# Kernel tuning notes

Measured on AMD Instinct MI355X. Metric: run time of the kernel, lower is better.

## Reference

```python
import math
import jax, jax.numpy as jnp
import numpy as np

B, CIN, Hh, Ww = 8, 3, 64, 64
D_MODEL = 512
N_STATE = 64
N2 = N_STATE // 2
N_LAYERS = 4
LATENT = 256
L = Hh * Ww  # 4096
EPS = 1e-5


def setup_inputs() -> dict:
    key = jax.random.key(0)
    ks = jax.random.split(key, 12)
    x = jax.random.normal(ks[0], (B, CIN, Hh, Ww), jnp.float32)
    Wproj = jax.random.normal(ks[1], (D_MODEL, CIN), jnp.float32) * (1.0 / math.sqrt(CIN))
    bproj = jnp.zeros((D_MODEL,), jnp.float32)
    pos_emb = jax.random.normal(ks[2], (1, L, D_MODEL), jnp.float32)
    # S4D kernel params (stacked over layers), per minimal S4D init
    log_dt = jax.random.uniform(ks[3], (N_LAYERS, D_MODEL), jnp.float32) * (math.log(0.1) - math.log(0.001)) + math.log(0.001)
    log_A_real = jnp.full((N_LAYERS, D_MODEL, N2), math.log(0.5), jnp.float32)
    A_imag = jnp.broadcast_to(math.pi * jnp.arange(N2, dtype=jnp.float32), (N_LAYERS, D_MODEL, N2)) + jnp.zeros((N_LAYERS, D_MODEL, N2), jnp.float32)
    C_re = jax.random.normal(ks[4], (N_LAYERS, D_MODEL, N2), jnp.float32) * (0.5 ** 0.5)
    C_im = jax.random.normal(ks[5], (N_LAYERS, D_MODEL, N2), jnp.float32) * (0.5 ** 0.5)
    Dskip = jax.random.normal(ks[6], (N_LAYERS, D_MODEL), jnp.float32)
    Wout = jax.random.normal(ks[7], (N_LAYERS, 2 * D_MODEL, D_MODEL), jnp.float32) * (1.0 / math.sqrt(D_MODEL))
    bout = jnp.zeros((N_LAYERS, 2 * D_MODEL), jnp.float32)
    ln_g = jnp.ones((N_LAYERS, D_MODEL), jnp.float32)
    ln_b = jnp.zeros((N_LAYERS, D_MODEL), jnp.float32)
    Wstats = jax.random.normal(ks[8], (2 * LATENT, D_MODEL), jnp.float32) * (1.0 / math.sqrt(D_MODEL))
    bstats = jnp.zeros((2 * LATENT,), jnp.float32)
    return dict(x=x, Wproj=Wproj, bproj=bproj, pos_emb=pos_emb, log_dt=log_dt,
                log_A_real=log_A_real, A_imag=A_imag, C_re=C_re, C_im=C_im,
                Dskip=Dskip, Wout=Wout, bout=bout, ln_g=ln_g, ln_b=ln_b,
                Wstats=Wstats, bstats=bstats)


def _s4d_layer(u, log_dt, log_A_real, A_imag, C_re, C_im, Dskip, Wout, bout):
    # u: (B, H, L); diagonal SSM via Vandermonde kernel + FFT conv (minimal S4D)
    Lseq = u.shape[-1]
    dt = jnp.exp(log_dt)                              # (H,)
    A = -jnp.exp(log_A_real) + 1j * A_imag            # (H, N2)
    dtA = A * dt[:, None]                             # (H, N2)
    Cc = (C_re + 1j * C_im) * (jnp.exp(dtA) - 1.0) / A
    t = jnp.arange(Lseq, dtype=jnp.float32)
    K = 2.0 * jnp.einsum('hn,hnl->hl', Cc, jnp.exp(dtA[:, :, None] * t)).real  # (H, L)
    k_f = jnp.fft.rfft(K, n=2 * Lseq)                 # (H, L+1)
    u_f = jnp.fft.rfft(u, n=2 * Lseq)                 # (B, H, L+1)
    y = jnp.fft.irfft(u_f * k_f, n=2 * Lseq)[..., :Lseq]
    y = y + u * Dskip[:, None]
    y = jax.nn.gelu(y, approximate=False)
    # 1x1 conv to 2H then GLU over channel dim
    y2 = jnp.einsum('oh,bhl->bol', Wout, y) + bout[:, None]
    a, b = jnp.split(y2, 2, axis=1)
    return a * jax.nn.sigmoid(b)


def _layernorm(x, g, b):
    # x: (B, L, H), normalize over H
    mu = jnp.mean(x, axis=-1, keepdims=True)
    var = jnp.mean((x - mu) ** 2, axis=-1, keepdims=True)
    return (x - mu) * jax.lax.rsqrt(var + EPS) * g + b


def reference(x, Wproj, bproj, pos_emb, log_dt, log_A_real, A_imag, C_re, C_im,
              Dskip, Wout, bout, ln_g, ln_b, Wstats, bstats):
    Bx = x.shape[0]
    # 1x1 Conv2d input projection
    h = jnp.einsum('oc,bchw->bohw', Wproj, x) + bproj[None, :, None, None]
    h = h.reshape(Bx, D_MODEL, L).transpose(0, 2, 1)  # (B, L, D)
    h = h + pos_emb
    h = h.transpose(0, 2, 1)                          # (B, D, L)
    for i in range(N_LAYERS):
        z = _s4d_layer(h, log_dt[i], log_A_real[i], A_imag[i], C_re[i], C_im[i],
                       Dskip[i], Wout[i], bout[i])
        h = h + z                                     # residual (dropout = identity at eval)
        h = _layernorm(h.transpose(0, 2, 1), ln_g[i], ln_b[i]).transpose(0, 2, 1)
    h = h.mean(-1)                                    # (B, D)
    stats = h @ Wstats.T + bstats
    mu, log_sig = jnp.split(stats, 2, axis=-1)
    return mu, log_sig
```

## Files before the change

### kernel.cpp

```cpp
#include <hip/hip_runtime.h>
#include <hip/hip_bf16.h>
#include <hip/hip_fp16.h>
#include <cmath>

#define BATCH   8
#define D_MODEL 512
#define N2      32
#define LSEQ    4096
#define NLAYERS 4
#define CIN     3
#define NBDL    (16777216u)
#define PN      (D_MODEL * N2)
#define WN      (2 * D_MODEL * D_MODEL)

typedef __attribute__((ext_vector_type(8))) short short8;
typedef __attribute__((ext_vector_type(4))) float floatx4;

__device__ float   g_h[NBDL];
__device__ __align__(16) __hip_bfloat16 g_yb[NBDL];
__device__ __align__(16) __hip_bfloat16 g_yt[NBDL];
__device__ __align__(16) __hip_bfloat16 g_wb[NLAYERS * WN];
__device__ __align__(16) __hip_bfloat16 g_G[(size_t)NLAYERS * 512 * 6 * 4096];
__device__ __align__(16) float g_posT[D_MODEL * LSEQ];
__device__ float4  g_p[NLAYERS * PN];
__device__ float   g_hm[BATCH * D_MODEL];
__device__ int     g_flag;

__device__ __forceinline__ float bfbits2f(unsigned short u) {
    union { unsigned int i; float f; } x; x.i = ((unsigned int)u) << 16; return x.f;
}
__device__ __forceinline__ float halfbits2f(unsigned short u) {
    __half h; *(unsigned short*)&h = u; return __half2float(h);
}
__device__ __forceinline__ float ldin(const void* p, size_t i, int m) {
    if (m == 1) return ((const float*)p)[i];
    unsigned short u = ((const unsigned short*)p)[i];
    if (m == 0) return bfbits2f(u);
    return halfbits2f(u);
}
__device__ __forceinline__ unsigned int pk2(float a, float b) {
    __hip_bfloat16 ha = __float2bfloat16(a), hb = __float2bfloat16(b);
    unsigned short ua, ub;
    __builtin_memcpy(&ua, &ha, 2); __builtin_memcpy(&ub, &hb, 2);
    return (unsigned int)ua | ((unsigned int)ub << 16);
}
__device__ __forceinline__ void split2(float a, float b, unsigned int& hp, unsigned int& lp) {
    __hip_bfloat16 ah = __float2bfloat16(a), bh = __float2bfloat16(b);
    unsigned short ua, ub;
    __builtin_memcpy(&ua, &ah, 2); __builtin_memcpy(&ub, &bh, 2);
    hp = (unsigned int)ua | ((unsigned int)ub << 16);
    lp = pk2(a - __bfloat162float(ah), b - __bfloat162float(bh));
}
__device__ __forceinline__ unsigned short bf16u(float a) {
    __hip_bfloat16 h = __float2bfloat16(a);
    unsigned short u; __builtin_memcpy(&u, &h, 2); return u;
}
__device__ __forceinline__ float2 cpow_(float br, float bi, int e) {
    float rr = 1.f, ri = 0.f;
    while (e) {
        if (e & 1) { float t = rr * br - ri * bi; ri = rr * bi + ri * br; rr = t; }
        float t = br * br - bi * bi; bi = 2.f * br * bi; br = t;
        e >>= 1;
    }
    return make_float2(rr, ri);
}

__device__ __forceinline__ float fast_gelu(float x) {
    float z = x * 0.70710678118654752f;
    float a = fabsf(z);
    float t = __builtin_amdgcn_rcpf(fmaf(0.3275911f, a, 1.0f));
    float p = t * fmaf(t, fmaf(t, fmaf(t, fmaf(t, 1.061405429f, -1.453152027f),
                                       1.421413741f), -0.284496736f), 0.254829592f);
    float e = __expf(-a * a);
    float er = fmaf(-p, e, 1.0f);
    er = copysignf(er, z);
    float hx = 0.5f * x;
    return fmaf(hx, er, hx);
}

__global__ void detect_kernel(const unsigned short* a) {
    if (threadIdx.x == 0) {
        unsigned short h1 = a[1], h3 = a[3];
        int f;
        if (h1 == 0x0000 && h3 == 0x4049) f = 1;
        else if (h1 == 0x4049)            f = 0;
        else if (h1 == 0x4248)            f = 2;
        else                              f = 1;
        g_flag = f;
    }
}

__global__ __launch_bounds__(256) void sentinel_kernel(float* out, float v) {
    out[blockIdx.x * 256 + threadIdx.x] = v;
}

__global__ __launch_bounds__(256) void pos_t_kernel(const void* pos) {
    __shared__ float T[64][65];
    const int m = g_flag;
    int tid = threadIdx.x;
    int bid = blockIdx.x;
    int l0 = (bid >> 3) * 64;
    int o0 = (bid & 7) * 64;
    int a  = tid & 63;
    int g4 = tid >> 6;
#pragma unroll
    for (int p = 0; p < 16; p++) {
        int ll = g4 * 16 + p;
        T[a][ll] = ldin(pos, (size_t)(l0 + ll) * D_MODEL + o0 + a, m);
    }
    __syncthreads();
#pragma unroll
    for (int p = 0; p < 16; p++) {
        int oo = g4 * 16 + p;
        g_posT[(size_t)(o0 + oo) * LSEQ + l0 + a] = T[oo][a];
    }
}

__global__ __launch_bounds__(256) void proj_kernel(const void* x, const void* Wproj,
                                                   const void* bproj) {
    const int m = g_flag;
    unsigned idx = blockIdx.x * 256 + threadIdx.x;
    int l = idx & (LSEQ - 1);
    int o = idx >> 12;
    float acc0 = ldin(bproj, o, m) + g_posT[(size_t)o * LSEQ + l];
    float w0 = ldin(Wproj, o * CIN + 0, m);
    float w1 = ldin(Wproj, o * CIN + 1, m);
    float w2 = ldin(Wproj, o * CIN + 2, m);
#pragma unroll
    for (int b = 0; b < BATCH; b++) {
        float acc = acc0;
        acc = fmaf(w0, ldin(x, (size_t)(b * CIN + 0) * LSEQ + l, m), acc);
        acc = fmaf(w1, ldin(x, (size_t)(b * CIN + 1) * LSEQ + l, m), acc);
        acc = fmaf(w2, ldin(x, (size_t)(b * CIN + 2) * LSEQ + l, m), acc);
        g_h[(size_t)(b * D_MODEL + o) * LSEQ + l] = acc;
    }
}

__global__ __launch_bounds__(256) void prep_kernel(const void* log_dt, const void* log_A_real,
                                                   const void* A_imag, const void* C_re,
                                                   const void* C_im) {
    const int m = g_flag;
    int idx = blockIdx.x * 256 + threadIdx.x;
    int layer = idx >> 14;
    int i = idx & (PN - 1);
    int hh = i >> 5;
    size_t oH = (size_t)layer * D_MODEL;
    size_t oN = (size_t)layer * PN;
    float dt  = expf(ldin(log_dt, oH + hh, m));
    float a   = expf(ldin(log_A_real, oN + i, m));
    float bi  = ldin(A_imag, oN + i, m);
    float dre = -a * dt, dim = bi * dt;
    float er  = expf(dre);
    float wr  = er * cosf(dim);
    float wi  = er * sinf(dim);
    float Er  = wr - 1.0f, Ei = wi;
    float inv = 1.0f / (a * a + bi * bi);
    float Tr = (-Er * a + Ei * bi) * inv;
    float Ti = -(Er * bi + Ei * a) * inv;
    float cr = ldin(C_re, oN + i, m), ci = ldin(C_im, oN + i, m);
    float c2r = 2.0f * (cr * Tr - ci * Ti);
    float c2i = 2.0f * (cr * Ti + ci * Tr);
    g_p[idx] = make_float4(wr, wi, c2r, c2i);
}

__global__ __launch_bounds__(256) void pack_w_kernel(const void* Wout) {
    int idx = blockIdx.x * 256 + threadIdx.x;
    g_wb[idx] = __float2bfloat16(ldin(Wout, idx, g_flag));
}

__global__ __launch_bounds__(256) void gmat_kernel() {
    __shared__ float4 psh[32];
    __shared__ unsigned short Khi[64], Klo[64];
    __shared__ __align__(16) unsigned short sC[2][64][72];
    float (*Kpart)[64] = (float(*)[64])&sC[0][0][0];
    int tid = threadIdx.x;
    int bid = blockIdx.x;
    int layer = bid >> 9, h = bid & 511;
    if (tid < 32) psh[tid] = g_p[(size_t)layer * PN + h * N2 + tid];
    __syncthreads();
    if (tid < 128) {
        int n = tid >> 2, dseg = (tid & 3) * 16;
        float4 pv = psh[n];
        float wr = pv.x, wi = pv.y;
        float2 wd = cpow_(wr, wi, dseg);
#pragma unroll
        for (int i = 0; i < 16; i++) {
            Kpart[n][dseg + i] = pv.z * wd.x - pv.w * wd.y;
            float t2 = wd.x * wr - wd.y * wi;
            wd.y = wd.x * wi + wd.y * wr; wd.x = t2;
        }
    }
    __syncthreads();
    if (tid < 64) {
        float acc = 0.f;
#pragma unroll
        for (int n = 0; n < 32; n++) acc += Kpart[n][tid];
        unsigned short khu = bf16u(acc);
        Khi[tid] = khu;
        Klo[tid] = bf16u(acc - bfbits2f(khu));
    }
    __syncthreads();
    unsigned short* Gu = (unsigned short*)(g_G + (size_t)bid * 6 * 4096);
    int t = tid >> 2, jseg = (tid & 3) * 16;
    {
        unsigned int mh[8], ml[8];
#pragma unroll
        for (int i2 = 0; i2 < 8; i2++) {
            int d0 = t - jseg - 2 * i2;
            int d1 = d0 - 1;
            unsigned int h0 = (d0 >= 0) ? (unsigned int)Khi[d0] : 0u;
            unsigned int h1 = (d1 >= 0) ? (unsigned int)Khi[d1] : 0u;
            unsigned int l0v = (d0 >= 0) ? (unsigned int)Klo[d0] : 0u;
            unsigned int l1v = (d1 >= 0) ? (unsigned int)Klo[d1] : 0u;
            mh[i2] = h0 | (h1 << 16);
            ml[i2] = l0v | (l1v << 16);
        }
        uint4 v;
        v.x = mh[0]; v.y = mh[1]; v.z = mh[2]; v.w = mh[3];
        *(uint4*)&Gu[t * 64 + jseg] = v;
        v.x = mh[4]; v.y = mh[5]; v.z = mh[6]; v.w = mh[7];
        *(uint4*)&Gu[t * 64 + jseg + 8] = v;
        v.x = ml[0]; v.y = ml[1]; v.z = ml[2]; v.w = ml[3];
        *(uint4*)&Gu[4096 + t * 64 + jseg] = v;
        v.x = ml[4]; v.y = ml[5]; v.z = ml[6]; v.w = ml[7];
        *(uint4*)&Gu[4096 + t * 64 + jseg + 8] = v;
    }
    {
        int n = t >> 1;
        float4 pv = psh[n];
        float wr = pv.x, wi = pv.y;
        float av[16];
        float2 wd = cpow_(wr, wi, 48 - jseg);
#pragma unroll
        for (int i = 15; i >= 0; i--) {
            av[i] = (t & 1) ? wd.y : wd.x;
            float t2 = wd.x * wr - wd.y * wi;
            wd.y = wd.x * wi + wd.y * wr; wd.x = t2;
        }
        unsigned int ah[8], al[8];
#pragma unroll
        for (int i2 = 0; i2 < 8; i2++)
            split2(av[2 * i2], av[2 * i2 + 1], ah[i2], al[i2]);
        uint4 v;
        v.x = ah[0]; v.y = ah[1]; v.z = ah[2]; v.w = ah[3];
        *(uint4*)&Gu[2 * 4096 + t * 64 + jseg] = v;
        v.x = ah[4]; v.y = ah[5]; v.z = ah[6]; v.w = ah[7];
        *(uint4*)&Gu[2 * 4096 + t * 64 + jseg + 8] = v;
        v.x = al[0]; v.y = al[1]; v.z = al[2]; v.w = al[3];
        *(uint4*)&Gu[3 * 4096 + t * 64 + jseg] = v;
        v.x = al[4]; v.y = al[5]; v.z = al[6]; v.w = al[7];
        *(uint4*)&Gu[3 * 4096 + t * 64 + jseg + 8] = v;
    }
    {
        int j = tid >> 2, tseg = (tid & 3) * 16;
        int n = j >> 1;
        float4 pv = psh[n];
        float wr = pv.x, wi = pv.y;
        float2 wd = cpow_(wr, wi, tseg + 1);
#pragma unroll
        for (int i = 0; i < 16; i++) {
            float zr = pv.z * wd.x - pv.w * wd.y;
            float zi = pv.z * wd.y + pv.w * wd.x;
            float cv = (j & 1) ? -zi : zr;
            unsigned short chu = bf16u(cv);
            sC[0][tseg + i][j] = chu;
            sC[1][tseg + i][j] = bf16u(cv - bfbits2f(chu));
            float t2 = wd.x * wr - wd.y * wi;
            wd.y = wd.x * wi + wd.y * wr; wd.x = t2;
        }
    }
    __syncthreads();
    *(uint4*)&Gu[4 * 4096 + t * 64 + jseg]     = *(uint4*)&sC[0][t][jseg];
    *(uint4*)&Gu[4 * 4096 + t * 64 + jseg + 8] = *(uint4*)&sC[0][t][jseg + 8];
    *(uint4*)&Gu[5 * 4096 + t * 64 + jseg]     = *(uint4*)&sC[1][t][jseg];
    *(uint4*)&Gu[5 * 4096 + t * 64 + jseg + 8] = *(uint4*)&sC[1][t][jseg + 8];
}

__global__ __launch_bounds__(256) void ssd_kernel(const void* Dskip, int layer) {
    __shared__ unsigned short sMhi[64][72];
    __shared__ unsigned short sMlo[64][72];
    __shared__ unsigned short sAC[64][72];
    __shared__ unsigned short sUhi[64][72];
    __shared__ unsigned short sUlo[64][72];
    __shared__ float sPf[64][68];
    const int m = g_flag;
    int tid = threadIdx.x;
    int h = blockIdx.x;
    const unsigned short* Gsrc = (const unsigned short*)g_G + (size_t)(layer * 512 + h) * 6 * 4096;

    int row = tid >> 2, seg = (tid & 3) * 16;

    {
        const unsigned short* s = Gsrc + row * 64 + seg;
        *(uint4*)&sMhi[row][seg]     = *(const uint4*)(s);
        *(uint4*)&sMhi[row][seg + 8] = *(const uint4*)(s + 8);
        *(uint4*)&sMlo[row][seg]     = *(const uint4*)(s + 4096);
        *(uint4*)&sMlo[row][seg + 8] = *(const uint4*)(s + 4096 + 8);
        *(uint4*)&sAC[row][seg]      = *(const uint4*)(s + 2 * 4096);
        *(uint4*)&sAC[row][seg + 8]  = *(const uint4*)(s + 2 * 4096 + 8);
    }
    {
        const float* up = g_h + (size_t)h * LSEQ + row * 64 + seg;
#pragma unroll
        for (int s8 = 0; s8 < 2; s8++) {
            float4 va = *(const float4*)(up + s8 * 8);
            float4 vb = *(const float4*)(up + s8 * 8 + 4);
            uint4 H, L;
            split2(va.x, va.y, H.x, L.x);
            split2(va.z, va.w, H.y, L.y);
            split2(vb.x, vb.y, H.z, L.z);
            split2(vb.z, vb.w, H.w, L.w);
            *(uint4*)&sUhi[row][seg + s8 * 8] = H;
            *(uint4*)&sUlo[row][seg + s8 * 8] = L;
        }
    }

    float sWr = 0.f, sWi = 0.f;
    if (tid < 32) {
        float4 pv = g_p[(size_t)layer * PN + h * N2 + tid];
        float Wr = pv.x, Wi = pv.y;
#pragma unroll
        for (int s6 = 0; s6 < 6; s6++) { float t2 = Wr * Wr - Wi * Wi; Wi = 2.f * Wr * Wi; Wr = t2; }
        sWr = Wr; sWi = Wi;
    }
    float dsk = ldin(Dskip, (size_t)layer * D_MODEL + h, m);

    int lane = tid & 63, wave = tid >> 6;
    int q = lane >> 4, nm = lane & 15;
    int cidx = wave * 16 + nm;
    floatx4 zed = {0.f, 0.f, 0.f, 0.f};

    for (int b = 0; b < 8; b++) {
        __syncthreads();
        float4 nu0, nu1, nu2, nu3;
        if (b < 7) {
            const float* up = g_h + (size_t)((b + 1) * D_MODEL + h) * LSEQ + row * 64 + seg;
            nu0 = *(const float4*)(up);
            nu1 = *(const float4*)(up + 4);
            nu2 = *(const float4*)(up + 8);
            nu3 = *(const float4*)(up + 12);
        }
        floatx4 pacc[4] = {zed, zed, zed, zed};
#pragma unroll
        for (int k0 = 0; k0 < 64; k0 += 32) {
            short8 bh = *(short8*)&sUhi[cidx][k0 + q * 8];
            short8 bl = *(short8*)&sUlo[cidx][k0 + q * 8];
#pragma unroll
            for (int mi = 0; mi < 4; mi++) {
                short8 a = *(short8*)&sAC[mi * 16 + nm][k0 + q * 8];
                pacc[mi] = __builtin_amdgcn_mfma_f32_16x16x32_bf16(a, bh, pacc[mi], 0, 0, 0);
                pacc[mi] = __builtin_amdgcn_mfma_f32_16x16x32_bf16(a, bl, pacc[mi], 0, 0, 0);
            }
        }
        __syncthreads();
        if (tid >= 128) {
            int idx = tid - 128, row2 = idx >> 1, seg2 = (idx & 1) * 32;
            const unsigned short* s = Gsrc + 3 * 4096 + row2 * 64 + seg2;
            *(uint4*)&sAC[row2][seg2]      = *(const uint4*)(s);
            *(uint4*)&sAC[row2][seg2 + 8]  = *(const uint4*)(s + 8);
            *(uint4*)&sAC[row2][seg2 + 16] = *(const uint4*)(s + 16);
            *(uint4*)&sAC[row2][seg2 + 24] = *(const uint4*)(s + 24);
        }
        __syncthreads();
#pragma unroll
        for (int k0 = 0; k0 < 64; k0 += 32) {
            short8 bh = *(short8*)&sUhi[cidx][k0 + q * 8];
#pragma unroll
            for (int mi = 0; mi < 4; mi++) {
                short8 a = *(short8*)&sAC[mi * 16 + nm][k0 + q * 8];
                pacc[mi] = __builtin_amdgcn_mfma_f32_16x16x32_bf16(a, bh, pacc[mi], 0, 0, 0);
            }
        }
#pragma unroll
        for (int mi = 0; mi < 4; mi++)
            *(floatx4*)&sPf[cidx][mi * 16 + q * 4] = pacc[mi];
        __syncthreads();

        if (tid < 32) {
            int n = tid;
            float Sr = 0.f, Si = 0.f;
            for (int c = 0; c < 64; c++) {
                unsigned int* wp = (unsigned int*)&sPf[c][0];
                unsigned int pru = wp[2 * n], piu = wp[2 * n + 1];
                float pr = __uint_as_float(pru), pi = __uint_as_float(piu);
                unsigned int shw, slw;
                split2(Sr, Si, shw, slw);
                wp[n]      = shw;
                wp[32 + n] = slw;
                float t2 = fmaf(sWr, Sr, fmaf(-sWi, Si, pr));
                Si = fmaf(sWr, Si, fmaf(sWi, Sr, pi));
                Sr = t2;
            }
        }
        if (tid >= 128) {
            int idx = tid - 128, row2 = idx >> 1, seg2 = (idx & 1) * 32;
            const unsigned short* s = Gsrc + 4 * 4096 + row2 * 64 + seg2;
            *(uint4*)&sAC[row2][seg2]      = *(const uint4*)(s);
            *(uint4*)&sAC[row2][seg2 + 8]  = *(const uint4*)(s + 8);
            *(uint4*)&sAC[row2][seg2 + 16] = *(const uint4*)(s + 16);
            *(uint4*)&sAC[row2][seg2 + 24] = *(const uint4*)(s + 24);
        }
        __syncthreads();

        floatx4 accA[4] = {zed, zed, zed, zed};
        floatx4 accB[4] = {zed, zed, zed, zed};
#pragma unroll
        for (int k0 = 0; k0 < 64; k0 += 32) {
            short8 bh = *(short8*)&sUhi[cidx][k0 + q * 8];
            short8 bl = *(short8*)&sUlo[cidx][k0 + q * 8];
            const unsigned short* srow = (const unsigned short*)&sPf[cidx][0];
            short8 sh = *(short8*)(srow + k0 + q * 8);
            short8 sl = *(short8*)(srow + 64 + k0 + q * 8);
#pragma unroll
            for (int mi = 0; mi < 4; mi++) {
                short8 amh = *(short8*)&sMhi[mi * 16 + nm][k0 + q * 8];
                short8 aml = *(short8*)&sMlo[mi * 16 + nm][k0 + q * 8];
                short8 ac  = *(short8*)&sAC [mi * 16 + nm][k0 + q * 8];
                accA[mi] = __builtin_amdgcn_mfma_f32_16x16x32_bf16(amh, bh, accA[mi], 0, 0, 0);
                accA[mi] = __builtin_amdgcn_mfma_f32_16x16x32_bf16(amh, bl, accA[mi], 0, 0, 0);
                accA[mi] = __builtin_amdgcn_mfma_f32_16x16x32_bf16(aml, bh, accA[mi], 0, 0, 0);
                accB[mi] = __builtin_amdgcn_mfma_f32_16x16x32_bf16(ac,  sh, accB[mi], 0, 0, 0);
                accB[mi] = __builtin_amdgcn_mfma_f32_16x16x32_bf16(ac,  sl, accB[mi], 0, 0, 0);
            }
        }
        __syncthreads();
        if (tid >= 128) {
            int idx = tid - 128, row2 = idx >> 1, seg2 = (idx & 1) * 32;
            const unsigned short* s = Gsrc + 5 * 4096 + row2 * 64 + seg2;
            *(uint4*)&sAC[row2][seg2]      = *(const uint4*)(s);
            *(uint4*)&sAC[row2][seg2 + 8]  = *(const uint4*)(s + 8);
            *(uint4*)&sAC[row2][seg2 + 16] = *(const uint4*)(s + 16);
            *(uint4*)&sAC[row2][seg2 + 24] = *(const uint4*)(s + 24);
        }
        __syncthreads();
#pragma unroll
        for (int k0 = 0; k0 < 64; k0 += 32) {
            const unsigned short* srow = (const unsigned short*)&sPf[cidx][0];
            short8 sh = *(short8*)(srow + k0 + q * 8);
#pragma unroll
            for (int mi = 0; mi < 4; mi++) {
                short8 ac = *(short8*)&sAC[mi * 16 + nm][k0 + q * 8];
                accB[mi] = __builtin_amdgcn_mfma_f32_16x16x32_bf16(ac, sh, accB[mi], 0, 0, 0);
            }
        }

        __hip_bfloat16* yb = g_yb + (size_t)(b * D_MODEL + h) * LSEQ;
#pragma unroll
        for (int mi = 0; mi < 4; mi++) {
            int t0 = mi * 16 + q * 4;
            uint2 uh = *(uint2*)&sUhi[cidx][t0];
            uint2 ul = *(uint2*)&sUlo[cidx][t0];
            float u0 = bfbits2f((unsigned short)(uh.x & 0xFFFF)) + bfbits2f((unsigned short)(ul.x & 0xFFFF));
            float u1 = bfbits2f((unsigned short)(uh.x >> 16))    + bfbits2f((unsigned short)(ul.x >> 16));
            float u2 = bfbits2f((unsigned short)(uh.y & 0xFFFF)) + bfbits2f((unsigned short)(ul.y & 0xFFFF));
            float u3 = bfbits2f((unsigned short)(uh.y >> 16))    + bfbits2f((unsigned short)(ul.y >> 16));
            float y0 = fast_gelu(accA[mi][0] + accB[mi][0] + dsk * u0);
            float y1 = fast_gelu(accA[mi][1] + accB[mi][1] + dsk * u1);
            float y2 = fast_gelu(accA[mi][2] + accB[mi][2] + dsk * u2);
            float y3 = fast_gelu(accA[mi][3] + accB[mi][3] + dsk * u3);
            uint2 o;
            o.x = pk2(y0, y1);
            o.y = pk2(y2, y3);
            *(uint2*)&yb[cidx * 64 + t0] = o;
        }
        __syncthreads();
        if (b < 7) {
            {
                const unsigned short* s = Gsrc + 2 * 4096 + row * 64 + seg;
                *(uint4*)&sAC[row][seg]     = *(const uint4*)(s);
                *(uint4*)&sAC[row][seg + 8] = *(const uint4*)(s + 8);
            }
            {
                uint4 H, L;
                split2(nu0.x, nu0.y, H.x, L.x);
                split2(nu0.z, nu0.w, H.y, L.y);
                split2(nu1.x, nu1.y, H.z, L.z);
                split2(nu1.z, nu1.w, H.w, L.w);
                *(uint4*)&sUhi[row][seg] = H;
                *(uint4*)&sUlo[row][seg] = L;
                split2(nu2.x, nu2.y, H.x, L.x);
                split2(nu2.z, nu2.w, H.y, L.y);
                split2(nu3.x, nu3.y, H.z, L.z);
                split2(nu3.z, nu3.w, H.w, L.w);
                *(uint4*)&sUhi[row][seg + 8] = H;
                *(uint4*)&sUlo[row][seg + 8] = L;
            }
        }
    }
}

__global__ __launch_bounds__(256, 4) void glu_mfma_kernel(const void* bout, int layer) {
    __shared__ __align__(16) unsigned char smem[25600];
    unsigned short (* __restrict__ Wa)[40] = (unsigned short(*)[40])(smem);
    unsigned short (* __restrict__ Wb)[40] = (unsigned short(*)[40])(smem + 2560);
    unsigned int*  __restrict__ Ytd        = (unsigned int*)(smem + 5120);
    unsigned short (* __restrict__ Zs)[264] = (unsigned short(*)[264])(smem);
    const int m = g_flag;
    int tid  = threadIdx.x;
    int wave = tid >> 6, lane = tid & 63;
    int q = lane >> 4, nm = lane & 15;
    int bid = blockIdx.x;
    int xcd = bid & 7;
    int qb  = bid >> 3;
    int rt  = qb & 15;
    int ct  = (xcd << 4) | (qb >> 4);
    int col0 = ct * 256;
    int row0 = rt * 32;
    int b  = col0 >> 12;
    int l0 = col0 & (LSEQ - 1);
    const unsigned short* __restrict__ Ybb =
        (const unsigned short*)g_yb + (size_t)b * D_MODEL * LSEQ;
    const __hip_bfloat16* __restrict__ Wbase = g_wb + (size_t)layer * WN;

    floatx4 accA[2][4], accB[2][4];
    floatx4 zed = {0.f, 0.f, 0.f, 0.f};
#pragma unroll
    for (int i = 0; i < 2; i++)
#pragma unroll
        for (int j = 0; j < 4; j++) { accA[i][j] = zed; accB[i][j] = zed; }

    int sk = (tid & 3) * 8;
    int wrow = (tid & 127) >> 2;
    int p  = tid >> 4;
    int sg = tid & 15;
    int Xw = (sg & 3) << 2;
    unsigned int rowbase = (unsigned)(sg * 16) * 20 + (unsigned)(p ^ Xw);
    int wavecol = wave * 64;

    for (int k0 = 0; k0 < D_MODEL; k0 += 32) {
        if (tid < 128)
            *(uint4*)&Wa[wrow][sk] = *(const uint4*)&Wbase[(size_t)(row0 + wrow) * D_MODEL + k0 + sk];
        else
            *(uint4*)&Wb[wrow][sk] = *(const uint4*)&Wbase[(size_t)(row0 + wrow + D_MODEL) * D_MODEL + k0 + sk];
        {
            const unsigned short* yA = Ybb + (size_t)(k0 + 2 * p) * LSEQ + l0 + sg * 16;
            uint4 a0 = *(const uint4*)yA;
            uint4 a1 = *(const uint4*)(yA + 8);
            uint4 b0 = *(const uint4*)(yA + LSEQ);
            uint4 b1 = *(const uint4*)(yA + LSEQ + 8);
#define PKW(au, bu, jj)  { \
            Ytd[rowbase + (jj) * 20]       = ((au) & 0xFFFFu) | ((bu) << 16); \
            Ytd[rowbase + ((jj) + 1) * 20] = ((au) >> 16) | ((bu) & 0xFFFF0000u); }
            PKW(a0.x, b0.x, 0)  PKW(a0.y, b0.y, 2)  PKW(a0.z, b0.z, 4)  PKW(a0.w, b0.w, 6)
            PKW(a1.x, b1.x, 8)  PKW(a1.y, b1.y, 10) PKW(a1.z, b1.z, 12) PKW(a1.w, b1.w, 14)
#undef PKW
        }
        __syncthreads();
        short8 afa[2], afb[2];
#pragma unroll
        for (int mi = 0; mi < 2; mi++) {
            afa[mi] = *(short8*)&Wa[mi * 16 + nm][q * 8];
            afb[mi] = *(short8*)&Wb[mi * 16 + nm][q * 8];
        }
#pragma unroll
        for (int ni = 0; ni < 4; ni++) {
            int r = wavecol + ni * 16 + nm;
            int Xr = ((r >> 4) & 3) << 2;
            short8 bf = *(short8*)(Ytd + r * 20 + ((q * 4) ^ Xr));
#pragma unroll
            for (int mi = 0; mi < 2; mi++) {
                accA[mi][ni] = __builtin_amdgcn_mfma_f32_16x16x32_bf16(afa[mi], bf, accA[mi][ni], 0, 0, 0);
                accB[mi][ni] = __builtin_amdgcn_mfma_f32_16x16x32_bf16(afb[mi], bf, accB[mi][ni], 0, 0, 0);
            }
        }
        __syncthreads();
    }

    size_t boff = (size_t)layer * 2 * D_MODEL;
#pragma unroll
    for (int mi = 0; mi < 2; mi++) {
#pragma unroll
        for (int r = 0; r < 4; r++) {
            int lrow = mi * 16 + q * 4 + r;
            int o = row0 + lrow;
            float ba  = ldin(bout, boff + o, m);
            float bb2 = ldin(bout, boff + o + D_MODEL, m);
#pragma unroll
            for (int ni = 0; ni < 4; ni++) {
                int lcol = wavecol + ni * 16 + nm;
                float aa = accA[mi][ni][r] + ba;
                float bv = accB[mi][ni][r] + bb2;
                float z  = aa * __builtin_amdgcn_rcpf(1.0f + __expf(-bv));
                __half hz = __float2half(z);
                unsigned short hzb;
                __builtin_memcpy(&hzb, &hz, 2);
                Zs[lrow][lcol] = hzb;
            }
        }
    }
    __syncthreads();
    unsigned short* __restrict__ Zb =
        (unsigned short*)g_yt + (size_t)b * D_MODEL * LSEQ;
    int zrow = tid >> 3;
    int zcol = (tid & 7) * 32;
    size_t gbase = (size_t)(row0 + zrow) * LSEQ + l0 + zcol;
#pragma unroll
    for (int i = 0; i < 4; i++)
        *(uint4*)&Zb[gbase + i * 8] = *(uint4*)&Zs[zrow][zcol + i * 8];
}

__global__ __launch_bounds__(256) void ln_kernel(const void* g, const void* bt, int layer) {
    __shared__ float s_sum[8][32];
    __shared__ float s_sq[8][32];
    __shared__ float s_mu[32], s_rs[32];
    const int m = g_flag;
    int tid = threadIdx.x;
    int l  = tid & 31;
    int dg = tid >> 5;
    int bl = blockIdx.x;
    int b  = bl >> 7;
    int l0 = (bl & 127) * 32;
    size_t base = (size_t)b * D_MODEL * LSEQ + l0 + l;
    float* __restrict__ hp = g_h + base + (size_t)(dg * 64) * LSEQ;
    const unsigned short* __restrict__ zp =
        (const unsigned short*)g_yt + base + (size_t)(dg * 64) * LSEQ;
    size_t goff = (size_t)layer * D_MODEL + dg * 64;
    float varr[64];
    float sum = 0.f, sq = 0.f;
#pragma unroll
    for (int i = 0; i < 64; i++) {
        float v = hp[(size_t)i * LSEQ] + halfbits2f(zp[(size_t)i * LSEQ]);
        varr[i] = v;
        sum += v; sq += v * v;
    }
    s_sum[dg][l] = sum; s_sq[dg][l] = sq;
    __syncthreads();
    if (tid < 32) {
        float s = 0.f, qq = 0.f;
#pragma unroll
        for (int gq = 0; gq < 8; gq++) { s += s_sum[gq][tid]; qq += s_sq[gq][tid]; }
        float mu = s * (1.0f / D_MODEL);
        float var = qq * (1.0f / D_MODEL) - mu * mu;
        s_mu[tid] = mu;
        s_rs[tid] = rsqrtf(var + 1e-5f);
    }
    __syncthreads();
    float mu = s_mu[l], rs = s_rs[l];
#pragma unroll
    for (int i = 0; i < 64; i++) {
        hp[(size_t)i * LSEQ] = (varr[i] - mu) * rs * ldin(g, goff + i, m) + ldin(bt, goff + i, m);
    }
}

__global__ __launch_bounds__(256) void mean_kernel() {
    int bd = blockIdx.x;
    int tid = threadIdx.x;
    const float* __restrict__ row = g_h + (size_t)bd * LSEQ;
    float s = 0.f;
    for (int l = tid; l < LSEQ; l += 256) s += row[l];
#pragma unroll
    for (int off = 32; off > 0; off >>= 1) s += __shfl_down(s, off, 64);
    __shared__ float red[4];
    if ((tid & 63) == 0) red[tid >> 6] = s;
    __syncthreads();
    if (tid == 0) g_hm[bd] = (red[0] + red[1] + red[2] + red[3]) * (1.0f / LSEQ);
}

__global__ __launch_bounds__(256) void stats_kernel(const void* Wst, const void* bst,
                                                    float* __restrict__ out) {
    const int m = g_flag;
    int idx = blockIdx.x * 256 + threadIdx.x;
    int b = idx >> 9, o = idx & (D_MODEL - 1);
    const float* __restrict__ hb = g_hm + b * D_MODEL;
    float acc = ldin(bst, o, m);
    for (int d = 0; d < D_MODEL; d++)
        acc = fmaf(hb[d], ldin(Wst, (size_t)o * D_MODEL + d, m), acc);
    int pos = (o < 256) ? (b * 256 + o) : (2048 + b * 256 + (o - 256));
    out[pos] = acc;
}

extern "C" void kernel_launch(void* const* d_in, const int* in_sizes, int n_in,
                              void* d_out, int out_size, void* d_ws, size_t ws_size,
                              hipStream_t stream) {
    static const int exp_sizes[16] = {98304, 1536, 512, 2097152, 2048, 65536, 65536,
                                      65536, 65536, 2048, 2097152, 4096, 2048, 2048,
                                      262144, 512};
    bool ok = (n_in == 16);
    if (ok) for (int i = 0; i < 16; i++) if (in_sizes[i] != exp_sizes[i]) { ok = false; break; }
    if (!ok) {
        sentinel_kernel<<<(out_size + 255) / 256, 256, 0, stream>>>((float*)d_out, 1000.0f);
        return;
    }
    if (out_size != 4096) {
        sentinel_kernel<<<(out_size + 255) / 256, 256, 0, stream>>>((float*)d_out, 300.0f);
        return;
    }

    const void* x          = d_in[0];
    const void* Wproj      = d_in[1];
    const void* bproj      = d_in[2];
    const void* pos        = d_in[3];
    const void* log_dt     = d_in[4];
    const void* log_A_real = d_in[5];
    const void* A_imag     = d_in[6];
    const void* C_re       = d_in[7];
    const void* C_im       = d_in[8];
    const void* Dskip      = d_in[9];
    const void* Wout       = d_in[10];
    const void* bout       = d_in[11];
    const void* ln_g       = d_in[12];
    const void* ln_b       = d_in[13];
    const void* Wstats     = d_in[14];
    const void* bstats     = d_in[15];

    detect_kernel<<<1, 64, 0, stream>>>((const unsigned short*)A_imag);
    pos_t_kernel<<<512, 256, 0, stream>>>(pos);
    proj_kernel<<<(D_MODEL * LSEQ) / 256, 256, 0, stream>>>(x, Wproj, bproj);
    prep_kernel<<<(NLAYERS * PN) / 256, 256, 0, stream>>>(
        log_dt, log_A_real, A_imag, C_re, C_im);
    pack_w_kernel<<<(NLAYERS * WN) / 256, 256, 0, stream>>>(Wout);
    gmat_kernel<<<NLAYERS * 512, 256, 0, stream>>>();

    for (int i = 0; i < NLAYERS; i++) {
        ssd_kernel<<<D_MODEL, 256, 0, stream>>>(Dskip, i);
        glu_mfma_kernel<<<2048, 256, 0, stream>>>(bout, i);
        ln_kernel<<<(BATCH * LSEQ) / 32, 256, 0, stream>>>(ln_g, ln_b, i);
    }

    mean_kernel<<<BATCH * D_MODEL, 256, 0, stream>>>();
    stats_kernel<<<(BATCH * D_MODEL) / 256, 256, 0, stream>>>(
        Wstats, bstats, (float*)d_out);
}
```

Baseline: 985.8 us.

## Double-buffer shared-memory tiles in GLU MFMA kernel to overlap loads with compute

The GLU GEMM loop now uses two shared-memory buffers. The next K-slice of weights and activations is staged while MFMAs run on the current slice, which removes one barrier per iteration and lets global-load latency hide behind compute. In exchange, shared memory per block doubles to 51200 bytes, the launch-bounds occupancy hint drops from 4 to 3 blocks, and the fully unrolled 16-iteration loop may raise register pressure and code size.

```diff
diff --git a/kernel.cpp b/kernel.cpp
--- a/kernel.cpp
+++ b/kernel.cpp
@@ -489,11 +489,8 @@
     }
 }
 
-__global__ __launch_bounds__(256, 4) void glu_mfma_kernel(const void* bout, int layer) {
-    __shared__ __align__(16) unsigned char smem[25600];
-    unsigned short (* __restrict__ Wa)[40] = (unsigned short(*)[40])(smem);
-    unsigned short (* __restrict__ Wb)[40] = (unsigned short(*)[40])(smem + 2560);
-    unsigned int*  __restrict__ Ytd        = (unsigned int*)(smem + 5120);
+__global__ __launch_bounds__(256, 3) void glu_mfma_kernel(const void* bout, int layer) {
+    __shared__ __align__(16) unsigned char smem[51200];
     unsigned short (* __restrict__ Zs)[264] = (unsigned short(*)[264])(smem);
     const int m = g_flag;
     int tid  = threadIdx.x;
@@ -527,44 +524,69 @@
     unsigned int rowbase = (unsigned)(sg * 16) * 20 + (unsigned)(p ^ Xw);
     int wavecol = wave * 64;
 
-    for (int k0 = 0; k0 < D_MODEL; k0 += 32) {
-        if (tid < 128)
-            *(uint4*)&Wa[wrow][sk] = *(const uint4*)&Wbase[(size_t)(row0 + wrow) * D_MODEL + k0 + sk];
-        else
-            *(uint4*)&Wb[wrow][sk] = *(const uint4*)&Wbase[(size_t)(row0 + wrow + D_MODEL) * D_MODEL + k0 + sk];
-        {
-            const unsigned short* yA = Ybb + (size_t)(k0 + 2 * p) * LSEQ + l0 + sg * 16;
-            uint4 a0 = *(const uint4*)yA;
-            uint4 a1 = *(const uint4*)(yA + 8);
-            uint4 b0 = *(const uint4*)(yA + LSEQ);
-            uint4 b1 = *(const uint4*)(yA + LSEQ + 8);
-#define PKW(au, bu, jj)  { \
-            Ytd[rowbase + (jj) * 20]       = ((au) & 0xFFFFu) | ((bu) << 16); \
-            Ytd[rowbase + ((jj) + 1) * 20] = ((au) >> 16) | ((bu) & 0xFFFF0000u); }
-            PKW(a0.x, b0.x, 0)  PKW(a0.y, b0.y, 2)  PKW(a0.z, b0.z, 4)  PKW(a0.w, b0.w, 6)
-            PKW(a1.x, b1.x, 8)  PKW(a1.y, b1.y, 10) PKW(a1.z, b1.z, 12) PKW(a1.w, b1.w, 14)
-#undef PKW
-        }
-        __syncthreads();
-        short8 afa[2], afb[2];
-#pragma unroll
-        for (int mi = 0; mi < 2; mi++) {
-            afa[mi] = *(short8*)&Wa[mi * 16 + nm][q * 8];
-            afb[mi] = *(short8*)&Wb[mi * 16 + nm][q * 8];
-        }
-#pragma unroll
-        for (int ni = 0; ni < 4; ni++) {
-            int r = wavecol + ni * 16 + nm;
-            int Xr = ((r >> 4) & 3) << 2;
-            short8 bf = *(short8*)(Ytd + r * 20 + ((q * 4) ^ Xr));
-#pragma unroll
-            for (int mi = 0; mi < 2; mi++) {
-                accA[mi][ni] = __builtin_amdgcn_mfma_f32_16x16x32_bf16(afa[mi], bf, accA[mi][ni], 0, 0, 0);
-                accB[mi][ni] = __builtin_amdgcn_mfma_f32_16x16x32_bf16(afb[mi], bf, accB[mi][ni], 0, 0, 0);
-            }
-        }
-        __syncthreads();
-    }
+#define STAGE(bb, kk) { \
+    unsigned short (*Wa_)[40] = (unsigned short(*)[40])(bb); \
+    unsigned short (*Wb_)[40] = (unsigned short(*)[40])((bb) + 2560); \
+    unsigned int*   Ytd_      = (unsigned int*)((bb) + 5120); \
+    if (tid < 128) \
+        *(uint4*)&Wa_[wrow][sk] = *(const uint4*)&Wbase[(size_t)(row0 + wrow) * D_MODEL + (kk) + sk]; \
+    else \
+        *(uint4*)&Wb_[wrow][sk] = *(const uint4*)&Wbase[(size_t)(row0 + wrow + D_MODEL) * D_MODEL + (kk) + sk]; \
+    const unsigned short* yA = Ybb + (size_t)((kk) + 2 * p) * LSEQ + l0 + sg * 16; \
+    uint4 a0 = *(const uint4*)yA; \
+    uint4 a1 = *(const uint4*)(yA + 8); \
+    uint4 b0 = *(const uint4*)(yA + LSEQ); \
+    uint4 b1 = *(const uint4*)(yA + LSEQ + 8); \
+    Ytd_[rowbase +  0 * 20] = (a0.x & 0xFFFFu) | (b0.x << 16); \
+    Ytd_[rowbase +  1 * 20] = (a0.x >> 16) | (b0.x & 0xFFFF0000u); \
+    Ytd_[rowbase +  2 * 20] = (a0.y & 0xFFFFu) | (b0.y << 16); \
+    Ytd_[rowbase +  3 * 20] = (a0.y >> 16) | (b0.y & 0xFFFF0000u); \
+    Ytd_[rowbase +  4 * 20] = (a0.z & 0xFFFFu) | (b0.z << 16); \
+    Ytd_[rowbase +  5 * 20] = (a0.z >> 16) | (b0.z & 0xFFFF0000u); \
+    Ytd_[rowbase +  6 * 20] = (a0.w & 0xFFFFu) | (b0.w << 16); \
+    Ytd_[rowbase +  7 * 20] = (a0.w >> 16) | (b0.w & 0xFFFF0000u); \
+    Ytd_[rowbase +  8 * 20] = (a1.x & 0xFFFFu) | (b1.x << 16); \
+    Ytd_[rowbase +  9 * 20] = (a1.x >> 16) | (b1.x & 0xFFFF0000u); \
+    Ytd_[rowbase + 10 * 20] = (a1.y & 0xFFFFu) | (b1.y << 16); \
+    Ytd_[rowbase + 11 * 20] = (a1.y >> 16) | (b1.y & 0xFFFF0000u); \
+    Ytd_[rowbase + 12 * 20] = (a1.z & 0xFFFFu) | (b1.z << 16); \
+    Ytd_[rowbase + 13 * 20] = (a1.z >> 16) | (b1.z & 0xFFFF0000u); \
+    Ytd_[rowbase + 14 * 20] = (a1.w & 0xFFFFu) | (b1.w << 16); \
+    Ytd_[rowbase + 15 * 20] = (a1.w >> 16) | (b1.w & 0xFFFF0000u); \
+}
+
+#define COMPUTE(bb) { \
+    unsigned short (*Wa_)[40] = (unsigned short(*)[40])(bb); \
+    unsigned short (*Wb_)[40] = (unsigned short(*)[40])((bb) + 2560); \
+    unsigned int*   Ytd_      = (unsigned int*)((bb) + 5120); \
+    short8 afa[2], afb[2]; \
+    afa[0] = *(short8*)&Wa_[nm][q * 8];        afb[0] = *(short8*)&Wb_[nm][q * 8]; \
+    afa[1] = *(short8*)&Wa_[16 + nm][q * 8];   afb[1] = *(short8*)&Wb_[16 + nm][q * 8]; \
+    _Pragma("unroll") \
+    for (int ni = 0; ni < 4; ni++) { \
+        int r = wavecol + ni * 16 + nm; \
+        int Xr = ((r >> 4) & 3) << 2; \
+        short8 bf = *(short8*)(Ytd_ + r * 20 + ((q * 4) ^ Xr)); \
+        _Pragma("unroll") \
+        for (int mi = 0; mi < 2; mi++) { \
+            accA[mi][ni] = __builtin_amdgcn_mfma_f32_16x16x32_bf16(afa[mi], bf, accA[mi][ni], 0, 0, 0); \
+            accB[mi][ni] = __builtin_amdgcn_mfma_f32_16x16x32_bf16(afb[mi], bf, accB[mi][ni], 0, 0, 0); \
+        } \
+    } \
+}
+
+    STAGE(smem, 0);
+    __syncthreads();
+#pragma unroll
+    for (int it = 0; it < 16; it++) {
+        unsigned char* cur = smem + (unsigned)(it & 1) * 25600u;
+        unsigned char* nxt = smem + (unsigned)((it + 1) & 1) * 25600u;
+        if (it < 15) STAGE(nxt, (it + 1) * 32);
+        COMPUTE(cur);
+        __syncthreads();
+    }
+#undef STAGE
+#undef COMPUTE
 
     size_t boff = (size_t)layer * 2 * D_MODEL;
 #pragma unroll
```

New measurement: 999.2 us. About the same (+1.4%).
